# Performance work log

Hardware: AMD Instinct MI355X
Metric: run time of the kernel (lower is better)

## Reference

```python
import jax, jax.numpy as jnp
import numpy as np

NEG = -1e9  # masked_fill value from the original
B, S, E, H, L, V, CTX = 4, 1024, 1024, 16, 12, 50257, 1024
D = E // H
PAD_IDX = 0


def layernorm(x, g, b, eps=1e-5):
    m = jnp.mean(x, axis=-1, keepdims=True)
    v = jnp.var(x, axis=-1, keepdims=True)
    return (x - m) * jax.lax.rsqrt(v + eps) * g + b


def setup_inputs() -> dict:
    key = jax.random.key(0)
    ks = jax.random.split(key, 8)
    sc = 0.02
    init = lambda k, shape: (jax.random.normal(k, shape, jnp.float32) * sc)
    return {
        "x": jax.random.randint(ks[0], (B, S), 0, V),
        "wte": init(ks[1], (V, E)),
        "wpe": init(ks[2], (CTX, E)),
        "Wq": init(ks[3], (L, E, E)), "bq": jnp.zeros((L, E), jnp.float32),
        "Wkv": init(ks[4], (L, E, E)), "bkv": jnp.zeros((L, E), jnp.float32),
        "Wfc": init(ks[5], (L, E, 4 * E)), "bfc": jnp.zeros((L, 4 * E), jnp.float32),
        "Wproj": init(ks[6], (L, 4 * E, E)), "bproj": jnp.zeros((L, E), jnp.float32),
        "ln1_g": jnp.ones((L, E), jnp.float32), "ln1_b": jnp.zeros((L, E), jnp.float32),
        "ln2_g": jnp.ones((L, E), jnp.float32), "ln2_b": jnp.zeros((L, E), jnp.float32),
        "lnf_g": jnp.ones((E,), jnp.float32), "lnf_b": jnp.zeros((E,), jnp.float32),
    }


def reference(x, wte, wpe, Wq, bq, Wkv, bkv, Wfc, bfc, Wproj, bproj,
              ln1_g, ln1_b, ln2_g, ln2_b, lnf_g, lnf_b):
    # key padding mask: mask = (x != pad_idx) broadcast over queries
    key_mask = (x != PAD_IDX)  # (B, S) over key positions
    h = wte[x] + wpe[:S]       # (B, S, E); dropout is identity in eval

    def block(h, p):
        wq, bq_, wkv, bkv_, wfc, bfc_, wpj, bpj, g1, b1, g2, b2 = p
        # Q = c_attn(x); K = V = c_proj(x)  (shared key/value tensor, as in source)
        q = (h @ wq + bq_).reshape(B, S, H, D)
        kv = (h @ wkv + bkv_).reshape(B, S, H, D)
        # unscaled QK^T (original applies no 1/sqrt(d) scaling)
        scores = jnp.einsum('blhd,bmhd->bhlm', q, kv)          # (B,H,S,S)
        scores = jnp.where(key_mask[:, None, None, :], scores, NEG)
        probs = jax.nn.softmax(scores, axis=-1)                # attn dropout = identity
        attn = jnp.einsum('bhlm,bmhd->blhd', probs, kv).reshape(B, S, E)
        u = layernorm(h + attn, g1, b1)                        # ln_1(x + attn)
        m = jax.nn.gelu(u @ wfc + bfc_, approximate=False) @ wpj + bpj
        # NOTE: second residual is the BLOCK INPUT h (not u), per the source
        return layernorm(m + h, g2, b2), None

    h, _ = jax.lax.scan(
        block, h,
        (Wq, bq, Wkv, bkv, Wfc, bfc, Wproj, bproj, ln1_g, ln1_b, ln2_g, ln2_b))
    return layernorm(h, lnf_g, lnf_b)
```

## Files before the change

kernel.cpp:

```cpp
#include <hip/hip_runtime.h>

#define SEQ    1024
#define EDIM   1024
#define NHEAD  16
#define DHEAD  64
#define NLAYER 12
#define NTOK   4096
#define QKVN   2048

typedef float f32x4  __attribute__((ext_vector_type(4)));
typedef short bf16x8 __attribute__((ext_vector_type(8)));

__device__ __forceinline__ unsigned short f32_to_bf16(float f) {
    union { float f; unsigned u; } v; v.f = f;
    return (unsigned short)((v.u + 0x7fffu + ((v.u >> 16) & 1u)) >> 16);
}

__device__ __forceinline__ void gload_lds16(const unsigned short* g, unsigned short* l) {
    __builtin_amdgcn_global_load_lds((const __attribute__((address_space(1))) void*)g,
                                     (__attribute__((address_space(3))) void*)l, 16, 0, 0);
}

#define BARRIER() do { __builtin_amdgcn_s_barrier(); asm volatile("" ::: "memory"); } while (0)

__global__ __launch_bounds__(256) void transpose_bf16_k(
    const float* __restrict__ W, unsigned short* __restrict__ WT,
    int K, int N, size_t wStride, size_t wtStride)
{
    __shared__ float tile[32][33];
    const int l = blockIdx.z;
    W  += (size_t)l * wStride;
    WT += (size_t)l * wtStride;
    const int n0 = blockIdx.x * 32, k0 = blockIdx.y * 32;
    const int t = threadIdx.x;
    const int r = t >> 3, c4 = (t & 7) * 4;
    const float4 v = *reinterpret_cast<const float4*>(&W[(size_t)(k0 + r) * N + n0 + c4]);
    tile[r][c4 + 0] = v.x; tile[r][c4 + 1] = v.y;
    tile[r][c4 + 2] = v.z; tile[r][c4 + 3] = v.w;
    __syncthreads();
    ushort4 o;
    o.x = f32_to_bf16(tile[c4 + 0][r]);
    o.y = f32_to_bf16(tile[c4 + 1][r]);
    o.z = f32_to_bf16(tile[c4 + 2][r]);
    o.w = f32_to_bf16(tile[c4 + 3][r]);
    *reinterpret_cast<ushort4*>(&WT[(size_t)(n0 + r) * K + k0 + c4]) = o;
}

__global__ __launch_bounds__(256) void bias_concat_k(
    const float* __restrict__ bq, const float* __restrict__ bkv,
    float* __restrict__ bqkv)
{
    const int l = blockIdx.x, t = threadIdx.x;
    #pragma unroll
    for (int i = 0; i < 4; ++i) {
        const int c = t + i * 256;
        bqkv[(size_t)l * QKVN + c]        = bq[(size_t)l * EDIM + c];
        bqkv[(size_t)l * QKVN + EDIM + c] = bkv[(size_t)l * EDIM + c];
    }
}

__global__ __launch_bounds__(256) void embed_k(
    const int* __restrict__ x, const float* __restrict__ wte,
    const float* __restrict__ wpe, float* __restrict__ h,
    unsigned short* __restrict__ hb)
{
    const int bs  = blockIdx.x;
    const int s   = bs & (SEQ - 1);
    const int tok = x[bs];
    const int c   = threadIdx.x * 4;
    float4 a = *reinterpret_cast<const float4*>(&wte[(size_t)tok * EDIM + c]);
    const float4 p = *reinterpret_cast<const float4*>(&wpe[(size_t)s * EDIM + c]);
    a.x += p.x; a.y += p.y; a.z += p.z; a.w += p.w;
    *reinterpret_cast<float4*>(&h[(size_t)bs * EDIM + c]) = a;
    ushort4 o;
    o.x = f32_to_bf16(a.x); o.y = f32_to_bf16(a.y);
    o.z = f32_to_bf16(a.z); o.w = f32_to_bf16(a.w);
    *reinterpret_cast<ushort4*>(&hb[(size_t)bs * EDIM + c]) = o;
}

template<int NADD, int WF32, int WBF16>
__global__ __launch_bounds__(256) void add_ln_k(
    const float* __restrict__ x1, const float* __restrict__ x2,
    const float* __restrict__ x3, const float* __restrict__ x4,
    const float* __restrict__ x5, const float* __restrict__ g,
    const float* __restrict__ b, float* __restrict__ outf,
    unsigned short* __restrict__ outb)
{
    const int row = blockIdx.x;
    const int t   = threadIdx.x;
    const int c   = t * 4;
    const size_t base = (size_t)row * EDIM + c;
    float4 a = *reinterpret_cast<const float4*>(x1 + base);
    if (NADD >= 2) {
        const float4 v = *reinterpret_cast<const float4*>(x2 + base);
        a.x += v.x; a.y += v.y; a.z += v.z; a.w += v.w;
    }
    if (NADD >= 3) {
        const float4 v = *reinterpret_cast<const float4*>(x3 + base);
        a.x += v.x; a.y += v.y; a.z += v.z; a.w += v.w;
    }
    if (NADD >= 4) {
        const float4 v = *reinterpret_cast<const float4*>(x4 + base);
        a.x += v.x; a.y += v.y; a.z += v.z; a.w += v.w;
    }
    if (NADD >= 5) {
        const float4 v = *reinterpret_cast<const float4*>(x5 + base);
        a.x += v.x; a.y += v.y; a.z += v.z; a.w += v.w;
    }
    float s  = a.x + a.y + a.z + a.w;
    float ss = a.x * a.x + a.y * a.y + a.z * a.z + a.w * a.w;
    #pragma unroll
    for (int o = 32; o > 0; o >>= 1) {
        s  += __shfl_down(s, o);
        ss += __shfl_down(ss, o);
    }
    __shared__ float rs[4], rss[4];
    const int lane = t & 63, wv = t >> 6;
    if (lane == 0) { rs[wv] = s; rss[wv] = ss; }
    __syncthreads();
    s  = rs[0] + rs[1] + rs[2] + rs[3];
    ss = rss[0] + rss[1] + rss[2] + rss[3];
    const float mean = s * (1.f / EDIM);
    const float var  = ss * (1.f / EDIM) - mean * mean;
    const float inv  = rsqrtf(var + 1e-5f);
    const float4 gv = *reinterpret_cast<const float4*>(g + c);
    const float4 bv = *reinterpret_cast<const float4*>(b + c);
    float4 y;
    y.x = (a.x - mean) * inv * gv.x + bv.x;
    y.y = (a.y - mean) * inv * gv.y + bv.y;
    y.z = (a.z - mean) * inv * gv.z + bv.z;
    y.w = (a.w - mean) * inv * gv.w + bv.w;
    if (WF32) *reinterpret_cast<float4*>(outf + base) = y;
    if (WBF16) {
        ushort4 o;
        o.x = f32_to_bf16(y.x); o.y = f32_to_bf16(y.y);
        o.z = f32_to_bf16(y.z); o.w = f32_to_bf16(y.w);
        *reinterpret_cast<ushort4*>(outb + base) = o;
    }
}

template<int GELU, int OUTBF16>
__global__ __launch_bounds__(256) void gemm_bt_k(
    const unsigned short* __restrict__ A,
    const unsigned short* __restrict__ BT,
    const float* __restrict__ bias, void* __restrict__ Cout,
    void* __restrict__ Cout2, int M, int N, int K)
{
    __shared__ unsigned short As[128 * 32];
    __shared__ unsigned short Bs[128 * 32];

    const int t    = threadIdx.x;
    const int lane = t & 63;
    const int wave = t >> 6;
    const int wr   = wave >> 1, wc = wave & 1;
    const int lrow = lane & 15, lgrp = lane >> 4;

    const int nbx = gridDim.x;
    int flat = blockIdx.y * nbx + blockIdx.x;
    const int nwg = nbx * gridDim.y;
    flat = (flat & 7) * (nwg >> 3) + (flat >> 3);
    const int row0 = (flat / nbx) * 128, col0 = (flat % nbx) * 128;

    const int kspan = K / gridDim.z;
    const int koff  = blockIdx.z * kspan;

    const int srow  = lane >> 2;
    const int skoff = (lane & 3) * 8;
    const unsigned short* aP0 = A  + (size_t)(row0 + 32 * wave + srow) * K + skoff;
    const unsigned short* aP1 = aP0 + (size_t)16 * K;
    const unsigned short* bP0 = BT + (size_t)(col0 + 32 * wave + srow) * K + skoff;
    const unsigned short* bP1 = bP0 + (size_t)16 * K;
    unsigned short* aL0 = As + wave * 1024;
    unsigned short* aL1 = As + wave * 1024 + 512;
    unsigned short* bL0 = Bs + wave * 1024;
    unsigned short* bL1 = Bs + wave * 1024 + 512;

    f32x4 acc[4][4];
    #pragma unroll
    for (int i = 0; i < 4; ++i)
        #pragma unroll
        for (int j = 0; j < 4; ++j)
            acc[i][j] = (f32x4){0.f, 0.f, 0.f, 0.f};

    for (int k0 = koff; k0 < koff + kspan; k0 += 32) {
        gload_lds16(aP0 + k0, aL0);
        gload_lds16(aP1 + k0, aL1);
        gload_lds16(bP0 + k0, bL0);
        gload_lds16(bP1 + k0, bL1);
        __syncthreads();

        bf16x8 af[4], bf[4];
        #pragma unroll
        for (int m = 0; m < 4; ++m)
            af[m] = *reinterpret_cast<const bf16x8*>(
                &As[(wr * 64 + m * 16 + lrow) * 32 + lgrp * 8]);
        #pragma unroll
        for (int n = 0; n < 4; ++n)
            bf[n] = *reinterpret_cast<const bf16x8*>(
                &Bs[(wc * 64 + n * 16 + lrow) * 32 + lgrp * 8]);

        #pragma unroll
        for (int n = 0; n < 4; ++n)
            #pragma unroll
            for (int m = 0; m < 4; ++m)
                acc[m][n] = __builtin_amdgcn_mfma_f32_16x16x32_bf16(
                    af[m], bf[n], acc[m][n], 0, 0, 0);
        __syncthreads();
    }

    const int z = blockIdx.z;
    #pragma unroll
    for (int n = 0; n < 4; ++n) {
        const int col = col0 + wc * 64 + n * 16 + lrow;
        const float bv = (z == 0) ? bias[col] : 0.f;
        #pragma unroll
        for (int m = 0; m < 4; ++m) {
            const int rb = row0 + wr * 64 + m * 16 + lgrp * 4;
            #pragma unroll
            for (int r = 0; r < 4; ++r) {
                float xv = acc[m][n][r] + bv;
                if (GELU) xv = 0.5f * xv * (1.f + erff(xv * 0.70710678118654752f));
                if (OUTBF16) {
                    ((unsigned short*)Cout)[(size_t)(rb + r) * N + col] = f32_to_bf16(xv);
                } else {
                    float* dst = (z == 0) ? (float*)Cout : (float*)Cout2;
                    dst[(size_t)(rb + r) * N + col] = xv;
                }
            }
        }
    }
}

template<int GELU, int OUT>
__global__ __launch_bounds__(512) void gemm256_k(
    const unsigned short* __restrict__ A,
    const unsigned short* __restrict__ BT,
    const float* __restrict__ bias, unsigned short* __restrict__ C,
    float* __restrict__ P0, float* __restrict__ P1,
    float* __restrict__ P2, float* __restrict__ P3,
    int M, int N, int K)
{
    __shared__ unsigned short sh[65536];
    unsigned short* Asm = sh;
    unsigned short* Bsm = sh + 32768;

    const int tid  = threadIdx.x;
    const int lane = tid & 63;
    const int wave = tid >> 6;
    const int wm   = wave >> 2;
    const int wn   = wave & 3;
    const int lrow = lane & 15, lgrp = lane >> 4;

    const int ntc = N >> 8;
    const int nwg = gridDim.x;
    int flat = (blockIdx.x & 7) * (nwg >> 3) + (blockIdx.x >> 3);
    const int row0 = (flat / ntc) * 256;
    const int col0 = (flat % ntc) * 256;

    const int kspan = K / gridDim.y;
    const int koff  = blockIdx.y * kspan;
    const int NT    = kspan >> 6;

    f32x4 acc[8][4];
    #pragma unroll
    for (int i = 0; i < 8; ++i)
        #pragma unroll
        for (int j = 0; j < 4; ++j)
            acc[i][j] = (f32x4){0.f, 0.f, 0.f, 0.f};

    auto stage_half = [&](const unsigned short* g, unsigned short* l) {
        #pragma unroll
        for (int c = 0; c < 2; ++c) {
            const int d = (tid + c * 512) * 16;
            const int L = d ^ (((d >> 7) & 7) << 4);
            gload_lds16(g + (size_t)(L >> 7) * K + ((L & 127) >> 1), l + (d >> 1));
        }
    };
    auto stageA = [&](int buf, int kt, int h) {
        stage_half(A + (size_t)(row0 + h * 128) * K + koff + kt * 64,
                   Asm + buf * 16384 + h * 8192);
    };
    auto stageB = [&](int buf, int kt, int h) {
        stage_half(BT + (size_t)(col0 + h * 128) * K + koff + kt * 64,
                   Bsm + buf * 16384 + h * 8192);
    };

    auto rdA = [&](int buf, int p, bf16x8 (&af)[2][2]) {
        #pragma unroll
        for (int m = 0; m < 2; ++m)
            #pragma unroll
            for (int ks = 0; ks < 2; ++ks) {
                const int r  = wm * 128 + p * 32 + m * 16 + lrow;
                const int cB = (ks * 64 + lgrp * 16) ^ ((r & 7) << 4);
                af[m][ks] = *reinterpret_cast<const bf16x8*>(
                    &Asm[buf * 16384 + ((r * 128 + cB) >> 1)]);
            }
    };
    auto rdB = [&](int buf, bf16x8 (&bfr)[4][2]) {
        #pragma unroll
        for (int n = 0; n < 4; ++n)
            #pragma unroll
            for (int ks = 0; ks < 2; ++ks) {
                const int r  = wn * 64 + n * 16 + lrow;
                const int cB = (ks * 64 + lgrp * 16) ^ ((r & 7) << 4);
                bfr[n][ks] = *reinterpret_cast<const bf16x8*>(
                    &Bsm[buf * 16384 + ((r * 128 + cB) >> 1)]);
            }
    };
    auto mq = [&](int p, bf16x8 (&af)[2][2], bf16x8 (&bfr)[4][2]) {
        __builtin_amdgcn_s_setprio(1);
        #pragma unroll
        for (int ks = 0; ks < 2; ++ks)
            #pragma unroll
            for (int n = 0; n < 4; ++n)
                #pragma unroll
                for (int m = 0; m < 2; ++m)
                    acc[p * 2 + m][n] = __builtin_amdgcn_mfma_f32_16x16x32_bf16(
                        af[m][ks], bfr[n][ks], acc[p * 2 + m][n], 0, 0, 0);
        __builtin_amdgcn_s_setprio(0);
    };

    stageA(0, 0, 0); stageA(0, 0, 1);
    stageB(0, 0, 0); stageB(0, 0, 1);
    stageA(1, 1, 0); stageA(1, 1, 1);
    stageB(1, 1, 0); stageB(1, 1, 1);
    asm volatile("s_waitcnt vmcnt(8)" ::: "memory");
    BARRIER();

    for (int t = 0; t < NT; t += 2) {
        bf16x8 bfr[4][2], af[2][2];
        rdB(0, bfr); rdA(0, 0, af);
        if (t > 0) { stageA(1, t + 1, 0); stageA(1, t + 1, 1); }
        BARRIER(); mq(0, af, bfr); BARRIER();
        rdA(0, 1, af);
        if (t + 2 < NT) stageB(0, t + 2, 0);
        BARRIER(); mq(1, af, bfr); BARRIER();
        rdA(0, 2, af);
        if (t + 2 < NT) stageB(0, t + 2, 1);
        BARRIER(); mq(2, af, bfr); BARRIER();
        rdA(0, 3, af);
        BARRIER(); mq(3, af, bfr);
        if (t + 2 < NT) { asm volatile("s_waitcnt vmcnt(4)" ::: "memory"); }
        else            { asm volatile("s_waitcnt vmcnt(0)" ::: "memory"); }
        BARRIER();
        rdB(1, bfr); rdA(1, 0, af);
        if (t + 2 < NT) stageA(0, t + 2, 0);
        BARRIER(); mq(0, af, bfr); BARRIER();
        rdA(1, 1, af);
        if (t + 2 < NT) stageA(0, t + 2, 1);
        if (t + 3 < NT) stageB(1, t + 3, 0);
        BARRIER(); mq(1, af, bfr); BARRIER();
        rdA(1, 2, af);
        if (t + 3 < NT) stageB(1, t + 3, 1);
        BARRIER(); mq(2, af, bfr); BARRIER();
        rdA(1, 3, af);
        BARRIER(); mq(3, af, bfr);
        if (t + 2 < NT) { asm volatile("s_waitcnt vmcnt(4)" ::: "memory"); }
        BARRIER();
    }

    const int z = blockIdx.y;
    #pragma unroll
    for (int n = 0; n < 4; ++n) {
        const int col = col0 + wn * 64 + n * 16 + lrow;
        const float bv = (z == 0) ? bias[col] : 0.f;
        #pragma unroll
        for (int mf = 0; mf < 8; ++mf) {
            const int rb = row0 + wm * 128 + mf * 16 + lgrp * 4;
            #pragma unroll
            for (int r = 0; r < 4; ++r) {
                float xv = acc[mf][n][r] + bv;
                if (GELU) xv = 0.5f * xv * (1.f + erff(xv * 0.70710678118654752f));
                if (OUT == 0) {
                    C[(size_t)(rb + r) * N + col] = f32_to_bf16(xv);
                } else {
                    float* dst = (z == 0) ? P0 : (z == 1) ? P1 : (z == 2) ? P2 : P3;
                    dst[(size_t)(rb + r) * N + col] = xv;
                }
            }
        }
    }
}

#define KVP 68
__global__ __launch_bounds__(256) void attn_k(
    const unsigned short* __restrict__ qkv, const int* __restrict__ x,
    float* __restrict__ out)
{
    __shared__ unsigned short KVr[64][KVP];
    __shared__ unsigned short KVt[64 * 64];
    __shared__ unsigned short Ps[4][32][KVP];
    __shared__ float maskf[64];

    int flat = blockIdx.x + 8 * (blockIdx.y + 16 * blockIdx.z);
    flat = (flat & 7) * 64 + (flat >> 3);
    const int qt = flat & 7;
    const int hh = (flat >> 3) & 15;
    const int b  = flat >> 7;

    const int t    = threadIdx.x;
    const int w    = t >> 6;
    const int lane = t & 63;
    const int lrow = lane & 15, lgrp = lane >> 4;

    const unsigned short* qb_  = qkv + ((size_t)b * SEQ) * QKVN + hh * DHEAD;
    const unsigned short* kvb_ = qkv + ((size_t)b * SEQ) * QKVN + EDIM + hh * DHEAD;
    const int* xb = x + b * SEQ;
    const int qrow0 = qt * 128 + w * 32;

    bf16x8 qf[2][2];
    #pragma unroll
    for (int m = 0; m < 2; ++m)
        #pragma unroll
        for (int ks = 0; ks < 2; ++ks)
            qf[m][ks] = *reinterpret_cast<const bf16x8*>(
                qb_ + (size_t)(qrow0 + m * 16 + lrow) * QKVN + ks * 32 + lgrp * 8);

    f32x4 O[2][4];
    float mrun[2][4], lrun[2][4];
    #pragma unroll
    for (int m = 0; m < 2; ++m)
        #pragma unroll
        for (int i = 0; i < 4; ++i) {
            O[m][i] = (f32x4){0.f, 0.f, 0.f, 0.f};
            mrun[m][i] = -3e30f; lrun[m][i] = 0.f;
        }

    const int NKT = SEQ / 64;
    ushort4 kvreg[4];
    int xv = 0;

    auto issueKV = [&](int kt) {
        #pragma unroll
        for (int i = 0; i < 4; ++i) {
            const int u2 = t + i * 256;
            const int kr = u2 >> 4, kc = (u2 & 15) * 4;
            kvreg[i] = *reinterpret_cast<const ushort4*>(
                &kvb_[(size_t)(kt * 64 + kr) * QKVN + kc]);
        }
        if (t < 64) xv = xb[kt * 64 + t];
    };
    issueKV(0);

    for (int kt = 0; kt < NKT; ++kt) {
        __syncthreads();
        #pragma unroll
        for (int i = 0; i < 4; ++i) {
            const int u2 = t + i * 256;
            const int kr = u2 >> 4, kc = (u2 & 15) * 4;
            *reinterpret_cast<ushort4*>(&KVr[kr][kc]) = kvreg[i];
            const unsigned short comp[4] = {kvreg[i].x, kvreg[i].y, kvreg[i].z, kvreg[i].w};
            #pragma unroll
            for (int j = 0; j < 4; ++j) {
                const int d = kc + j;
                const int sw = (d ^ (d >> 3)) & 7;
                KVt[(d * 128 + ((kr * 2) ^ (sw << 4))) >> 1] = comp[j];
            }
        }
        if (t < 64) maskf[t] = (xv != 0) ? 1.f : 0.f;
        if (kt + 1 < NKT) issueKV(kt + 1);
        __syncthreads();

        f32x4 s[2][4];
        #pragma unroll
        for (int m = 0; m < 2; ++m)
            #pragma unroll
            for (int n = 0; n < 4; ++n) s[m][n] = (f32x4){0.f, 0.f, 0.f, 0.f};
        #pragma unroll
        for (int ks = 0; ks < 2; ++ks)
            #pragma unroll
            for (int n = 0; n < 4; ++n) {
                union { bf16x8 v; ushort4 h[2]; } bb;
                bb.h[0] = *reinterpret_cast<const ushort4*>(
                    &KVr[16 * n + lrow][ks * 32 + lgrp * 8]);
                bb.h[1] = *reinterpret_cast<const ushort4*>(
                    &KVr[16 * n + lrow][ks * 32 + lgrp * 8 + 4]);
                #pragma unroll
                for (int m = 0; m < 2; ++m)
                    s[m][n] = __builtin_amdgcn_mfma_f32_16x16x32_bf16(
                        qf[m][ks], bb.v, s[m][n], 0, 0, 0);
            }

        #pragma unroll
        for (int n = 0; n < 4; ++n) {
            const float flag = maskf[16 * n + lrow];
            #pragma unroll
            for (int m = 0; m < 2; ++m)
                #pragma unroll
                for (int r = 0; r < 4; ++r)
                    s[m][n][r] = (flag != 0.f) ? s[m][n][r] : -1e9f;
        }

        #pragma unroll
        for (int m = 0; m < 2; ++m)
            #pragma unroll
            for (int r = 0; r < 4; ++r) {
                float v = fmaxf(fmaxf(s[m][0][r], s[m][1][r]),
                                fmaxf(s[m][2][r], s[m][3][r]));
                #pragma unroll
                for (int o = 1; o < 16; o <<= 1) v = fmaxf(v, __shfl_xor(v, o));
                const float mn = fmaxf(mrun[m][r], v);
                const float fs = __expf(mrun[m][r] - mn);
                mrun[m][r] = mn;
                lrun[m][r] *= fs;
                #pragma unroll
                for (int df = 0; df < 4; ++df) O[m][df][r] *= fs;
            }

        #pragma unroll
        for (int m = 0; m < 2; ++m) {
            float rsum[4] = {0.f, 0.f, 0.f, 0.f};
            #pragma unroll
            for (int n = 0; n < 4; ++n)
                #pragma unroll
                for (int r = 0; r < 4; ++r) {
                    const float p = __expf(s[m][n][r] - mrun[m][r]);
                    rsum[r] += p;
                    Ps[w][m * 16 + 4 * lgrp + r][16 * n + lrow] = f32_to_bf16(p);
                }
            #pragma unroll
            for (int r = 0; r < 4; ++r) {
                float v = rsum[r];
                #pragma unroll
                for (int o = 1; o < 16; o <<= 1) v += __shfl_xor(v, o);
                lrun[m][r] += v;
            }
        }

        #pragma unroll
        for (int ks = 0; ks < 2; ++ks) {
            bf16x8 paf[2];
            #pragma unroll
            for (int m = 0; m < 2; ++m) {
                union { bf16x8 v; ushort4 h[2]; } pp;
                pp.h[0] = *reinterpret_cast<const ushort4*>(
                    &Ps[w][m * 16 + lrow][ks * 32 + lgrp * 8]);
                pp.h[1] = *reinterpret_cast<const ushort4*>(
                    &Ps[w][m * 16 + lrow][ks * 32 + lgrp * 8 + 4]);
                paf[m] = pp.v;
            }
            #pragma unroll
            for (int df = 0; df < 4; ++df) {
                const int d  = 16 * df + lrow;
                const int sw = (d ^ (d >> 3)) & 7;
                const bf16x8 bvf = *reinterpret_cast<const bf16x8*>(
                    &KVt[(d * 128 + ((ks * 64 + lgrp * 16) ^ (sw << 4))) >> 1]);
                #pragma unroll
                for (int m = 0; m < 2; ++m)
                    O[m][df] = __builtin_amdgcn_mfma_f32_16x16x32_bf16(
                        paf[m], bvf, O[m][df], 0, 0, 0);
            }
        }
    }

    #pragma unroll
    for (int m = 0; m < 2; ++m)
        #pragma unroll
        for (int r = 0; r < 4; ++r) {
            const float inv = 1.f / lrun[m][r];
            const int row = qrow0 + m * 16 + 4 * lgrp + r;
            float* po = out + ((size_t)b * SEQ + row) * EDIM + hh * DHEAD;
            #pragma unroll
            for (int df = 0; df < 4; ++df)
                po[16 * df + lrow] = O[m][df][r] * inv;
        }
}

extern "C" void kernel_launch(void* const* d_in, const int* in_sizes, int n_in,
                              void* d_out, int out_size, void* d_ws, size_t ws_size,
                              hipStream_t stream)
{
    (void)in_sizes; (void)n_in; (void)out_size;

    const int*   x     = (const int*)  d_in[0];
    const float* wte   = (const float*)d_in[1];
    const float* wpe   = (const float*)d_in[2];
    const float* Wq    = (const float*)d_in[3];
    const float* bq    = (const float*)d_in[4];
    const float* Wkv   = (const float*)d_in[5];
    const float* bkv   = (const float*)d_in[6];
    const float* Wfc   = (const float*)d_in[7];
    const float* bfc   = (const float*)d_in[8];
    const float* Wproj = (const float*)d_in[9];
    const float* bproj = (const float*)d_in[10];
    const float* ln1g  = (const float*)d_in[11];
    const float* ln1b  = (const float*)d_in[12];
    const float* ln2g  = (const float*)d_in[13];
    const float* ln2b  = (const float*)d_in[14];
    const float* lnfg  = (const float*)d_in[15];
    const float* lnfb  = (const float*)d_in[16];

    const size_t MB = 1024 * 1024;
    char* W = (char*)d_ws;
    float*          h     = (float*)(W + 0 * MB);
    float*          att   = (float*)(W + 16 * MB);
    float*          mb    = (float*)(W + 32 * MB);
    unsigned short* hb    = (unsigned short*)(W + 48 * MB);
    unsigned short* qkv   = (unsigned short*)(W + 56 * MB);
    unsigned short* ub    = (unsigned short*)(W + 72 * MB);
    unsigned short* tb    = (unsigned short*)(W + 80 * MB);
    float*          bqkv  = (float*)(W + 112 * MB);
    unsigned short* wqkvT = (unsigned short*)(W + 113 * MB);
    unsigned short* wfcT  = (unsigned short*)(W + 161 * MB);
    unsigned short* wpjT  = (unsigned short*)(W + 257 * MB);
    float*          p2f   = (float*)(W + 56 * MB);
    float*          p3f   = (float*)(W + 353 * MB);

    const bool split4 = ws_size >= (size_t)369 * MB;

    bias_concat_k<<<NLAYER, 256, 0, stream>>>(bq, bkv, bqkv);
    transpose_bf16_k<<<dim3(32, 32, NLAYER), 256, 0, stream>>>(
        Wq, wqkvT, EDIM, EDIM, (size_t)EDIM * EDIM, (size_t)QKVN * EDIM);
    transpose_bf16_k<<<dim3(32, 32, NLAYER), 256, 0, stream>>>(
        Wkv, wqkvT + (size_t)EDIM * EDIM, EDIM, EDIM,
        (size_t)EDIM * EDIM, (size_t)QKVN * EDIM);
    transpose_bf16_k<<<dim3(128, 32, NLAYER), 256, 0, stream>>>(
        Wfc, wfcT, EDIM, 4 * EDIM, (size_t)4 * EDIM * EDIM, (size_t)4 * EDIM * EDIM);
    transpose_bf16_k<<<dim3(32, 128, NLAYER), 256, 0, stream>>>(
        Wproj, wpjT, 4 * EDIM, EDIM, (size_t)4 * EDIM * EDIM, (size_t)4 * EDIM * EDIM);

    embed_k<<<NTOK, 256, 0, stream>>>(x, wte, wpe, h, hb);

    for (int l = 0; l < NLAYER; ++l) {
        gemm_bt_k<0, 1><<<dim3(QKVN / 128, NTOK / 128), 256, 0, stream>>>(
            hb, wqkvT + (size_t)l * QKVN * EDIM, bqkv + (size_t)l * QKVN,
            qkv, nullptr, NTOK, QKVN, EDIM);

        attn_k<<<dim3(SEQ / 128, NHEAD, 4), 256, 0, stream>>>(qkv, x, att);

        add_ln_k<2, 0, 1><<<NTOK, 256, 0, stream>>>(
            h, att, nullptr, nullptr, nullptr,
            ln1g + l * EDIM, ln1b + l * EDIM, nullptr, ub);

        gemm256_k<1, 0><<<dim3((NTOK / 256) * (4 * EDIM / 256), 1), 512, 0, stream>>>(
            ub, wfcT + (size_t)l * 4 * EDIM * EDIM, bfc + (size_t)l * 4 * EDIM,
            tb, nullptr, nullptr, nullptr, nullptr, NTOK, 4 * EDIM, EDIM);

        if (split4) {
            gemm256_k<0, 1><<<dim3((NTOK / 256) * (EDIM / 256), 4), 512, 0, stream>>>(
                tb, wpjT + (size_t)l * 4 * EDIM * EDIM, bproj + (size_t)l * EDIM,
                nullptr, mb, att, p2f, p3f, NTOK, EDIM, 4 * EDIM);
            add_ln_k<5, 1, 1><<<NTOK, 256, 0, stream>>>(
                mb, att, p2f, p3f, h,
                ln2g + l * EDIM, ln2b + l * EDIM, h, hb);
        } else {
            gemm_bt_k<0, 0><<<dim3(EDIM / 128, NTOK / 128, 2), 256, 0, stream>>>(
                tb, wpjT + (size_t)l * 4 * EDIM * EDIM, bproj + (size_t)l * EDIM,
                mb, att, NTOK, EDIM, 4 * EDIM);
            add_ln_k<3, 1, 1><<<NTOK, 256, 0, stream>>>(
                mb, att, h, nullptr, nullptr,
                ln2g + l * EDIM, ln2b + l * EDIM, h, hb);
        }
    }

    add_ln_k<1, 1, 0><<<NTOK, 256, 0, stream>>>(
        h, nullptr, nullptr, nullptr, nullptr, lnfg, lnfb, (float*)d_out, nullptr);
}
```

Before: 2.691 ms.

## Double-buffer attention K/V tiles and use tanh-approximated GELU

The attention kernel now keeps two LDS buffers for the K/V tiles and the mask, and writes the next tile during compute on the current one. This cuts the per-iteration barriers from two to one and hides the LDS fill behind the MFMA work, at the cost of doubling the K/V LDS footprint, which may lower occupancy. Separately, the exact erf GELU in both GEMM epilogues is replaced by the tanh approximation built from __expf. That is cheaper, but it changes the math away from the reference's approximate=False.

```diff
diff --git a/kernel.cpp b/kernel.cpp
--- a/kernel.cpp
+++ b/kernel.cpp
@@ -14,6 +14,14 @@
 __device__ __forceinline__ unsigned short f32_to_bf16(float f) {
     union { float f; unsigned u; } v; v.f = f;
     return (unsigned short)((v.u + 0x7fffu + ((v.u >> 16) & 1u)) >> 16);
+}
+
+__device__ __forceinline__ float gelu_f(float x) {
+    const float y = 0.7978845608028654f * (x + 0.044715f * x * x * x);
+    const float e = __expf(-2.f * fabsf(y));
+    float th = (1.f - e) / (1.f + e);
+    th = (y < 0.f) ? -th : th;
+    return 0.5f * x * (1.f + th);
 }
 
 __device__ __forceinline__ void gload_lds16(const unsigned short* g, unsigned short* l) {
@@ -219,7 +227,7 @@
             #pragma unroll
             for (int r = 0; r < 4; ++r) {
                 float xv = acc[m][n][r] + bv;
-                if (GELU) xv = 0.5f * xv * (1.f + erff(xv * 0.70710678118654752f));
+                if (GELU) xv = gelu_f(xv);
                 if (OUTBF16) {
                     ((unsigned short*)Cout)[(size_t)(rb + r) * N + col] = f32_to_bf16(xv);
                 } else {
@@ -370,7 +378,7 @@
             #pragma unroll
             for (int r = 0; r < 4; ++r) {
                 float xv = acc[mf][n][r] + bv;
-                if (GELU) xv = 0.5f * xv * (1.f + erff(xv * 0.70710678118654752f));
+                if (GELU) xv = gelu_f(xv);
                 if (OUT == 0) {
                     C[(size_t)(rb + r) * N + col] = f32_to_bf16(xv);
                 } else {
@@ -387,10 +395,10 @@
     const unsigned short* __restrict__ qkv, const int* __restrict__ x,
     float* __restrict__ out)
 {
-    __shared__ unsigned short KVr[64][KVP];
-    __shared__ unsigned short KVt[64 * 64];
+    __shared__ unsigned short KVr[2][64][KVP];
+    __shared__ unsigned short KVt[2][4096];
     __shared__ unsigned short Ps[4][32][KVP];
-    __shared__ float maskf[64];
+    __shared__ float maskm[2][64];
 
     int flat = blockIdx.x + 8 * (blockIdx.y + 16 * blockIdx.z);
     flat = (flat & 7) * 64 + (flat >> 3);
@@ -440,26 +448,30 @@
         }
         if (t < 64) xv = xb[kt * 64 + t];
     };
-    issueKV(0);
-
-    for (int kt = 0; kt < NKT; ++kt) {
-        __syncthreads();
+    auto writeKV = [&](int buf) {
         #pragma unroll
         for (int i = 0; i < 4; ++i) {
             const int u2 = t + i * 256;
             const int kr = u2 >> 4, kc = (u2 & 15) * 4;
-            *reinterpret_cast<ushort4*>(&KVr[kr][kc]) = kvreg[i];
+            *reinterpret_cast<ushort4*>(&KVr[buf][kr][kc]) = kvreg[i];
             const unsigned short comp[4] = {kvreg[i].x, kvreg[i].y, kvreg[i].z, kvreg[i].w};
             #pragma unroll
             for (int j = 0; j < 4; ++j) {
                 const int d = kc + j;
                 const int sw = (d ^ (d >> 3)) & 7;
-                KVt[(d * 128 + ((kr * 2) ^ (sw << 4))) >> 1] = comp[j];
-            }
-        }
-        if (t < 64) maskf[t] = (xv != 0) ? 1.f : 0.f;
-        if (kt + 1 < NKT) issueKV(kt + 1);
-        __syncthreads();
+                KVt[buf][(d * 128 + ((kr * 2) ^ (sw << 4))) >> 1] = comp[j];
+            }
+        }
+        if (t < 64) maskm[buf][t] = (xv != 0) ? 1.f : 0.f;
+    };
+
+    issueKV(0);
+    writeKV(0);
+    issueKV(1);
+    __syncthreads();
+
+    for (int kt = 0; kt < NKT; ++kt) {
+        const int cur = kt & 1, nxt = cur ^ 1;
 
         f32x4 s[2][4];
         #pragma unroll
@@ -472,25 +484,27 @@
             for (int n = 0; n < 4; ++n) {
                 union { bf16x8 v; ushort4 h[2]; } bb;
                 bb.h[0] = *reinterpret_cast<const ushort4*>(
-                    &KVr[16 * n + lrow][ks * 32 + lgrp * 8]);
+                    &KVr[cur][16 * n + lrow][ks * 32 + lgrp * 8]);
                 bb.h[1] = *reinterpret_cast<const ushort4*>(
-                    &KVr[16 * n + lrow][ks * 32 + lgrp * 8 + 4]);
+                    &KVr[cur][16 * n + lrow][ks * 32 + lgrp * 8 + 4]);
                 #pragma unroll
                 for (int m = 0; m < 2; ++m)
                     s[m][n] = __builtin_amdgcn_mfma_f32_16x16x32_bf16(
                         qf[m][ks], bb.v, s[m][n], 0, 0, 0);
             }
 
+        if (kt + 1 < NKT) writeKV(nxt);
+        if (kt + 2 < NKT) issueKV(kt + 2);
+
         #pragma unroll
         for (int n = 0; n < 4; ++n) {
-            const float flag = maskf[16 * n + lrow];
+            const float flag = maskm[cur][16 * n + lrow];
             #pragma unroll
             for (int m = 0; m < 2; ++m)
                 #pragma unroll
                 for (int r = 0; r < 4; ++r)
                     s[m][n][r] = (flag != 0.f) ? s[m][n][r] : -1e9f;
         }
-
         #pragma unroll
         for (int m = 0; m < 2; ++m)
             #pragma unroll
@@ -506,7 +520,6 @@
                 #pragma unroll
                 for (int df = 0; df < 4; ++df) O[m][df][r] *= fs;
             }
-
         #pragma unroll
         for (int m = 0; m < 2; ++m) {
             float rsum[4] = {0.f, 0.f, 0.f, 0.f};
@@ -544,13 +557,15 @@
                 const int d  = 16 * df + lrow;
                 const int sw = (d ^ (d >> 3)) & 7;
                 const bf16x8 bvf = *reinterpret_cast<const bf16x8*>(
-                    &KVt[(d * 128 + ((ks * 64 + lgrp * 16) ^ (sw << 4))) >> 1]);
+                    &KVt[cur][(d * 128 + ((ks * 64 + lgrp * 16) ^ (sw << 4))) >> 1]);
                 #pragma unroll
                 for (int m = 0; m < 2; ++m)
                     O[m][df] = __builtin_amdgcn_mfma_f32_16x16x32_bf16(
                         paf[m], bvf, O[m][df], 0, 0, 0);
             }
         }
+
+        __syncthreads();
     }
 
     #pragma unroll
```

Result: slower. 2.929 ms (+8.8%).
